# Kernel optimization log

Hardware: AMD Instinct MI355X
Metric: run time of the kernel (lower is better)

Reference implementation:

```python
import jax, jax.numpy as jnp
import numpy as np

DEPTH = 6; HEADS = 6; DIM = 384; HD = DIM // HEADS
WS = 14; WINDOW_BLOCKS = (0, 1, 3, 4)
IMG = 512; PATCH = 16; GRID = IMG // PATCH        # 32x32 token grid
PRE_GRID = 14                                      # 224 // 16 pretrain grid
SCALE = HD ** -0.5


def layer_norm(x, w, b, eps=1e-5):
    u = x.mean(-1, keepdims=True)
    s = ((x - u) ** 2).mean(-1, keepdims=True)
    return (x - u) / jnp.sqrt(s + eps) * w + b


def get_rel_pos(size, rel_pos):
    # q_size == k_size here; relative coords in [0, 2*size-2]
    coords = jnp.arange(size)[:, None] - jnp.arange(size)[None, :] + (size - 1)
    return rel_pos[coords]  # (size, size, HD)


def attention(x, qkv_w, qkv_b, proj_w, proj_b, rel_h, rel_w):
    B, H, W, C = x.shape
    N = H * W
    qkv = (x.reshape(B, N, C) @ qkv_w.T + qkv_b).reshape(B, N, 3, HEADS, HD)
    qkv = jnp.moveaxis(qkv, 2, 0).transpose(0, 1, 3, 2, 4)  # (3,B,h,N,d)
    q, k, v = qkv[0], qkv[1], qkv[2]
    attn = jnp.einsum('bhqd,bhkd->bhqk', q * SCALE, k)
    # decomposed relative position bias (ViTDet add_decomposed_rel_pos)
    Rh = get_rel_pos(H, rel_h)  # (H,H,d)
    Rw = get_rel_pos(W, rel_w)  # (W,W,d)
    rq = q.reshape(B, HEADS, H, W, HD)
    bias_h = jnp.einsum('bnhwc,hkc->bnhwk', rq, Rh)  # (B,h,H,W,H)
    bias_w = jnp.einsum('bnhwc,wkc->bnhwk', rq, Rw)  # (B,h,H,W,W)
    attn = (attn.reshape(B, HEADS, H, W, H, W)
            + bias_h[..., :, None] + bias_w[..., None, :]).reshape(B, HEADS, N, N)
    attn = jax.nn.softmax(attn, axis=-1)
    out = jnp.einsum('bhqk,bhkd->bhqd', attn, v)
    out = out.transpose(0, 2, 1, 3).reshape(B, H, W, C)
    return out @ proj_w.T + proj_b


def window_partition(x, ws):
    B, H, W, C = x.shape
    pad_h = (ws - H % ws) % ws
    pad_w = (ws - W % ws) % ws
    x = jnp.pad(x, ((0, 0), (0, pad_h), (0, pad_w), (0, 0)))
    Hp, Wp = H + pad_h, W + pad_w
    x = x.reshape(B, Hp // ws, ws, Wp // ws, ws, C)
    x = x.transpose(0, 1, 3, 2, 4, 5).reshape(-1, ws, ws, C)
    return x, Hp, Wp


def window_unpartition(win, ws, Hp, Wp, H, W):
    B = win.shape[0] // ((Hp // ws) * (Wp // ws))
    x = win.reshape(B, Hp // ws, Wp // ws, ws, ws, -1)
    x = x.transpose(0, 1, 3, 2, 4, 5).reshape(B, Hp, Wp, -1)
    return x[:, :H, :W]


def block(x, p, windowed):
    shortcut = x
    x = layer_norm(x, p['n1w'], p['n1b'])
    if windowed:
        H, W = x.shape[1], x.shape[2]
        x, Hp, Wp = window_partition(x, WS)
    x = attention(x, p['qw'], p['qb'], p['pw'], p['pb'], p['rh'], p['rw'])
    if windowed:
        x = window_unpartition(x, WS, Hp, Wp, H, W)
    x = shortcut + x
    h = layer_norm(x, p['n2w'], p['n2b'])
    h = jax.nn.gelu(h @ p['f1w'].T + p['f1b'], approximate=False)
    return x + h @ p['f2w'].T + p['f2b']


def vit_forward(x, patch_w, patch_b, pos_embed, norm1_w, norm1_b, qkv_w, qkv_b,
                proj_w, proj_b, norm2_w, norm2_b, fc1_w, fc1_b, fc2_w, fc2_b,
                rel_pos_h, rel_pos_w):
    y = jax.lax.conv_general_dilated(
        x, patch_w, (PATCH, PATCH), 'VALID',
        dimension_numbers=('NCHW', 'OIHW', 'NCHW'))
    y = y.transpose(0, 2, 3, 1) + patch_b  # (B, GRID, GRID, DIM)
    # abs pos embed: bicubic resize from pretrain 14x14 grid to 32x32
    pos = pos_embed.reshape(1, PRE_GRID, PRE_GRID, DIM)
    pos = jax.image.resize(pos, (1, GRID, GRID, DIM), 'bicubic')
    y = y + pos
    for i in range(DEPTH):
        windowed = i in WINDOW_BLOCKS
        L = 2 * WS - 1 if windowed else 2 * GRID - 1
        p = dict(n1w=norm1_w[i], n1b=norm1_b[i], qw=qkv_w[i], qb=qkv_b[i],
                 pw=proj_w[i], pb=proj_b[i], rh=rel_pos_h[i, :L], rw=rel_pos_w[i, :L],
                 n2w=norm2_w[i], n2b=norm2_b[i], f1w=fc1_w[i], f1b=fc1_b[i],
                 f2w=fc2_w[i], f2b=fc2_b[i])
        y = block(y, p, windowed)
    return y.transpose(0, 3, 1, 2)  # (B, DIM, GRID, GRID) 'last_feat'


def setup_inputs() -> dict:
    key = jax.random.key(0)
    ks = jax.random.split(key, 10)
    B = 4
    std = 0.02
    f32 = jnp.float32
    return {
        'x': jax.random.normal(ks[0], (B, 3, IMG, IMG), f32),
        'patch_w': jax.random.normal(ks[1], (DIM, 3, PATCH, PATCH), f32) * 0.05,
        'patch_b': jnp.zeros((DIM,), f32),
        'pos_embed': jax.random.normal(ks[2], (1, PRE_GRID * PRE_GRID, DIM), f32) * std,
        'norm1_w': jnp.ones((DEPTH, DIM), f32),
        'norm1_b': jnp.zeros((DEPTH, DIM), f32),
        'qkv_w': jax.random.normal(ks[3], (DEPTH, 3 * DIM, DIM), f32) * std,
        'qkv_b': jnp.zeros((DEPTH, 3 * DIM), f32),
        'proj_w': jax.random.normal(ks[4], (DEPTH, DIM, DIM), f32) * std,
        'proj_b': jnp.zeros((DEPTH, DIM), f32),
        'norm2_w': jnp.ones((DEPTH, DIM), f32),
        'norm2_b': jnp.zeros((DEPTH, DIM), f32),
        'fc1_w': jax.random.normal(ks[5], (DEPTH, 4 * DIM, DIM), f32) * std,
        'fc1_b': jnp.zeros((DEPTH, 4 * DIM), f32),
        'fc2_w': jax.random.normal(ks[6], (DEPTH, DIM, 4 * DIM), f32) * std,
        'fc2_b': jnp.zeros((DEPTH, DIM), f32),
        'rel_pos_h': jax.random.normal(ks[7], (DEPTH, 2 * GRID - 1, HD), f32) * std,
        'rel_pos_w': jax.random.normal(ks[8], (DEPTH, 2 * GRID - 1, HD), f32) * std,
    }


def reference(x, patch_w, patch_b, pos_embed, norm1_w, norm1_b, qkv_w, qkv_b,
              proj_w, proj_b, norm2_w, norm2_b, fc1_w, fc1_b, fc2_w, fc2_b,
              rel_pos_h, rel_pos_w):
    return vit_forward(x, patch_w, patch_b, pos_embed, norm1_w, norm1_b, qkv_w, qkv_b,
                       proj_w, proj_b, norm2_w, norm2_b, fc1_w, fc1_b, fc2_w, fc2_b,
                       rel_pos_h, rel_pos_w)
```

## Files before the change

kernel.cpp:

```cpp
#include <hip/hip_runtime.h>
#include <math.h>

#define B_SZ 4
#define DIM 384
#define HEADS 6
#define HD 64
#define NTOK 4096
#define WS 14
#define NWIN 36
#define WTOK 196

typedef unsigned short u16;
typedef __bf16 bf16_t;
typedef bf16_t bf16x8 __attribute__((ext_vector_type(8)));
typedef float f32x4 __attribute__((ext_vector_type(4)));

__device__ __forceinline__ float bf2f(unsigned u) { return __uint_as_float(u << 16); }
__device__ __forceinline__ u16 f2bf(float f) {
    unsigned u = __float_as_uint(f);
    unsigned r = (u + 0x7fffu + ((u >> 16) & 1u)) >> 16;
    return (u16)r;
}

__device__ __forceinline__ void ldsload16(const u16* g, u16* l) {
    __builtin_amdgcn_global_load_lds(
        (const __attribute__((address_space(1))) unsigned int*)g,
        (__attribute__((address_space(3))) unsigned int*)l, 16, 0, 0);
}

__device__ __forceinline__ int swz(int r) { return (r ^ (r >> 2)) & 3; }

__device__ inline float cubic_keys(float x) {
    x = fabsf(x);
    if (x <= 1.f) return ((1.5f * x - 2.5f) * x) * x + 1.f;
    if (x < 2.f)  return ((-0.5f * x + 2.5f) * x - 4.f) * x + 2.f;
    return 0.f;
}

__global__ __launch_bounds__(256) void setup_kernel(
        const float* __restrict__ p0, const float* __restrict__ p1,
        const float* __restrict__ p2, const float* __restrict__ p3,
        const float* __restrict__ p4, const float* __restrict__ p5,
        u16* __restrict__ wb, const float* __restrict__ pe,
        float* __restrict__ posr, const float* __restrict__ x,
        u16* __restrict__ col) {
    int i = blockIdx.x * 256 + threadIdx.x;
    if (i < 10918656) {
        const float* s; int off;
        if      (i <   294912) { s = p0; off = 0; }
        else if (i <  2949120) { s = p1; off = 294912; }
        else if (i <  3833856) { s = p2; off = 2949120; }
        else if (i <  7372800) { s = p3; off = 3833856; }
        else if (i < 10911744) { s = p4; off = 7372800; }
        else                   { s = p5; off = 10911744; }
        wb[i] = f2bf(s[i - off]);
        return;
    }
    i -= 10918656;
    if (i < 393216) {
        int c = i % 384;
        int g = i / 384;
        int gy = g / 32, gx = g % 32;
        float wy[14], wx[14];
        float sy = (gy + 0.5f) * (14.f / 32.f) - 0.5f;
        float sx = (gx + 0.5f) * (14.f / 32.f) - 0.5f;
        float toty = 0.f, totx = 0.f;
        #pragma unroll
        for (int k = 0; k < 14; ++k) {
            wy[k] = cubic_keys(sy - (float)k); toty += wy[k];
            wx[k] = cubic_keys(sx - (float)k); totx += wx[k];
        }
        float val = 0.f;
        #pragma unroll 1
        for (int iy = 0; iy < 14; ++iy) {
            if (wy[iy] == 0.f) continue;
            float row = 0.f;
            for (int ix = 0; ix < 14; ++ix) {
                if (wx[ix] == 0.f) continue;
                row += wx[ix] * pe[(iy * 14 + ix) * 384 + c];
            }
            val += wy[iy] * row;
        }
        posr[i] = val / (toty * totx);
        return;
    }
    i -= 393216;
    {
        int kk = i % 768;
        int p  = i / 768;
        int b  = p / 1024;
        int ph = (p % 1024) / 32;
        int pw = p % 32;
        int c = kk / 256;
        int r = kk % 256;
        int ii = r / 16, j = r % 16;
        col[i] = f2bf(x[(size_t)b * 3 * 512 * 512 + (size_t)c * 512 * 512 +
                        (size_t)(ph * 16 + ii) * 512 + (pw * 16 + j)]);
    }
}

__global__ __launch_bounds__(64) void epi_ln_kernel(const float* __restrict__ P,
        const float* __restrict__ bias, const float* __restrict__ posr,
        float* __restrict__ y, int addy, int nsk,
        const float* __restrict__ lw, const float* __restrict__ lb,
        u16* __restrict__ lnout, float* __restrict__ outT)
{
    int tok = blockIdx.x, t = threadIdx.x;
    size_t base = (size_t)tok * 384;
    float v[6];
    float s = 0.f;
    #pragma unroll
    for (int i = 0; i < 6; ++i) {
        int c = t + 64 * i;
        float val = bias[c];
        #pragma unroll 1
        for (int sk = 0; sk < nsk; ++sk)
            val += P[(size_t)sk * 1572864 + base + c];
        if (posr) val += posr[(size_t)(tok & 1023) * 384 + c];
        if (addy) val += y[base + c];
        v[i] = val; s += val;
    }
    if (outT) {
        int b = tok >> 10, g = tok & 1023;
        #pragma unroll
        for (int i = 0; i < 6; ++i) {
            int c = t + 64 * i;
            outT[((size_t)(b * 384 + c)) * 1024 + g] = v[i];
        }
        return;
    }
    #pragma unroll
    for (int i = 0; i < 6; ++i) y[base + t + 64 * i] = v[i];
    if (!lnout) return;
    #pragma unroll
    for (int off = 32; off > 0; off >>= 1) s += __shfl_xor(s, off);
    float mean = s * (1.f / 384.f);
    float vs = 0.f;
    #pragma unroll
    for (int i = 0; i < 6; ++i) { float d = v[i] - mean; vs += d * d; }
    #pragma unroll
    for (int off = 32; off > 0; off >>= 1) vs += __shfl_xor(vs, off);
    float inv = rsqrtf(vs * (1.f / 384.f) + 1e-5f);
    u16* orow = lnout + base;
    #pragma unroll
    for (int i = 0; i < 6; ++i) {
        int c = t + 64 * i;
        orow[c] = f2bf((v[i] - mean) * inv * lw[c] + lb[c]);
    }
}

__global__ __launch_bounds__(256) void mfma_gemm3(
        const u16* __restrict__ A, const u16* __restrict__ Wt,
        const float* __restrict__ bias,
        float* __restrict__ outf, u16* __restrict__ outb,
        float* __restrict__ outp,
        int M, int N, int K, int act, int ksplit)
{
    __shared__ u16 As[8192];
    __shared__ u16 Bs[4096];
    int t = threadIdx.x;
    int lane = t & 63, wave = t >> 6;
    int wm = (wave >> 1) * 64, wn = (wave & 1) * 32;
    int m0 = blockIdx.y * 128, n0 = blockIdx.x * 64;
    int ks = blockIdx.z * ksplit, ke = ks + ksplit;

    int r0 = t >> 2,        c0 = ((t & 3) ^ swz(t >> 2)) * 8;
    int r1 = 64 + (t >> 2), c1 = ((t & 3) ^ swz(64 + (t >> 2))) * 8;
    const u16* a0 = A + (size_t)(m0 + r0) * K + c0;
    const u16* a1 = A + (size_t)(m0 + r1) * K + c1;
    const u16* b0 = Wt + (size_t)(n0 + r0) * K + c0;
    u16* asd0 = &As[wave * 512];
    u16* asd1 = &As[2048 + wave * 512];
    u16* bsd0 = &Bs[wave * 512];

    f32x4 acc[4][2] = {};
    int row_a = wm + (lane & 15);
    int row_b = wn + (lane & 15);
    int lq = lane >> 4;

    for (int k0 = ks; k0 < ke; k0 += 64) {
        ldsload16(a0 + k0, asd0);
        ldsload16(a1 + k0, asd1);
        ldsload16(b0 + k0, bsd0);
        ldsload16(a0 + k0 + 32, asd0 + 4096);
        ldsload16(a1 + k0 + 32, asd1 + 4096);
        ldsload16(b0 + k0 + 32, bsd0 + 2048);
        __syncthreads();
        #pragma unroll
        for (int hf = 0; hf < 2; ++hf) {
            bf16x8 af[4], bfr[2];
            #pragma unroll
            for (int i = 0; i < 4; ++i) {
                int r = row_a + i * 16;
                af[i] = *(const bf16x8*)&As[hf * 4096 + r * 32 + ((lq ^ swz(r)) * 8)];
            }
            #pragma unroll
            for (int j = 0; j < 2; ++j) {
                int r = row_b + j * 16;
                bfr[j] = *(const bf16x8*)&Bs[hf * 2048 + r * 32 + ((lq ^ swz(r)) * 8)];
            }
            #pragma unroll
            for (int i = 0; i < 4; ++i)
                #pragma unroll
                for (int j = 0; j < 2; ++j)
                    acc[i][j] = __builtin_amdgcn_mfma_f32_16x16x32_bf16(
                        af[i], bfr[j], acc[i][j], 0, 0, 0);
        }
        __syncthreads();
    }

    int colq = lane & 15, rowq = (lane >> 4) * 4;
    if (outp) {
        float* pp = outp + (size_t)blockIdx.z * M * N;
        #pragma unroll
        for (int i = 0; i < 4; ++i) {
            #pragma unroll
            for (int rr = 0; rr < 4; ++rr) {
                int m = m0 + wm + i * 16 + rowq + rr;
                size_t mo = (size_t)m * N;
                #pragma unroll
                for (int j = 0; j < 2; ++j) {
                    int n = n0 + wn + j * 16 + colq;
                    pp[mo + n] = acc[i][j][rr];
                }
            }
        }
        return;
    }
    #pragma unroll
    for (int i = 0; i < 4; ++i) {
        #pragma unroll
        for (int rr = 0; rr < 4; ++rr) {
            int m = m0 + wm + i * 16 + rowq + rr;
            size_t mo = (size_t)m * N;
            #pragma unroll
            for (int j = 0; j < 2; ++j) {
                int n = n0 + wn + j * 16 + colq;
                float v = acc[i][j][rr] + bias[n];
                if (act)  v = 0.5f * v * (1.f + erff(v * 0.70710678118654752f));
                if (outf) outf[mo + n] = v;
                if (outb) outb[mo + n] = f2bf(v);
            }
        }
    }
}

template<int N, int W>
__global__ __launch_bounds__(256) void attn_mfma(const u16* __restrict__ qkv,
        const u16* __restrict__ qkb, const float* __restrict__ rh,
        const float* __restrict__ rw, u16* __restrict__ outb)
{
    constexpr int JS = (W == 32) ? 64 : 32;
    constexpr int L  = (W == 32) ? 63 : 27;
    constexpr int CTR = W - 1;
    __shared__ u16 KV[11776];
    __shared__ u16 bhl[64 * 66];
    __shared__ u16 bwl[64 * 66];
    __shared__ u16 Qt[64 * 66];

    u16* Pb = KV + 9216;
    u16* Rt = KV;

    int t = threadIdx.x, lane = t & 63, wave = t >> 6;
    int quad = lane >> 4, l15 = lane & 15;
    int uh = blockIdx.x, qb0 = blockIdx.y * 64;
    int h = uh % HEADS, u = uh / HEADS;
    size_t tbase = (size_t)u * 1024;
    int wb_ = u / 9, wr = u - wb_ * 9;
    int wy = wr / 3, wx = wr - wy * 3;

    auto rowptr = [&](int lq2) -> const u16* {
        if constexpr (W == 32) {
            return qkv + (tbase + lq2) * 1152;
        } else {
            int iy = lq2 / WS, ix = lq2 - iy * WS;
            int gy = wy * WS + iy, gx = wx * WS + ix;
            if (gy < 32 && gx < 32)
                return qkv + (size_t)(wb_ * 1024 + gy * 32 + gx) * 1152;
            return qkb;
        }
    };

    {
        int q = t & 63, ch0 = (t >> 6) * 16;
        int qc = qb0 + q; if (qc >= N) qc = N - 1;
        const u16* qp = rowptr(qc) + h * 64 + ch0;
        uint4 a = *(const uint4*)qp;
        uint4 b = *(const uint4*)(qp + 8);
        u16 vals[16];
        *(uint4*)vals = a; *(uint4*)(vals + 8) = b;
        #pragma unroll
        for (int c = 0; c < 16; ++c)
            Qt[(ch0 + c) * 66 + q] = ((qb0 + q) < N) ? vals[c] : (u16)0;
    }

    #pragma unroll
    for (int table = 0; table < 2; ++table) {
        __syncthreads();
        const float* tab = table ? rw : rh;
        for (int idx = t; idx < JS * 8; idx += 256) {
            int j = idx >> 3, cc0 = (idx & 7) * 8;
            u16 tmp[8];
            if (j < L) {
                const float* src = tab + (size_t)j * 64 + cc0;
                #pragma unroll
                for (int c = 0; c < 8; ++c) tmp[c] = f2bf(src[c]);
            } else {
                #pragma unroll
                for (int c = 0; c < 8; ++c) tmp[c] = 0;
            }
            *(uint4*)&Rt[j * 72 + cc0] = *(uint4*)tmp;
        }
        __syncthreads();
        if (wave < JS / 16) {
            int jt = wave;
            bf16x8 af0 = *(const bf16x8*)&Rt[(jt * 16 + l15) * 72 + quad * 8];
            bf16x8 af1 = *(const bf16x8*)&Rt[(jt * 16 + l15) * 72 + 32 + quad * 8];
            u16* dst = table ? bwl : bhl;
            #pragma unroll
            for (int qt = 0; qt < 4; ++qt) {
                bf16x8 qf0, qf1;
                u16* p0 = (u16*)&qf0; u16* p1 = (u16*)&qf1;
                #pragma unroll
                for (int z = 0; z < 8; ++z) {
                    p0[z] = Qt[(quad * 8 + z) * 66 + qt * 16 + l15];
                    p1[z] = Qt[(32 + quad * 8 + z) * 66 + qt * 16 + l15];
                }
                f32x4 acc = {};
                acc = __builtin_amdgcn_mfma_f32_16x16x32_bf16(af0, qf0, acc, 0, 0, 0);
                acc = __builtin_amdgcn_mfma_f32_16x16x32_bf16(af1, qf1, acc, 0, 0, 0);
                #pragma unroll
                for (int r = 0; r < 4; ++r)
                    dst[(qt * 16 + l15) * 66 + jt * 16 + quad * 4 + r] = f2bf(acc[r]);
            }
        }
    }
    __syncthreads();

    constexpr int NKT = (N + 31) / 32;
    {
        int pch = wave * 64 + lane;
        int key = pch >> 3;
        int c8 = (pch & 7) ^ (key & 7);
        int kc = key; if (kc >= N) kc = N - 1;
        ldsload16(rowptr(kc) + 384 + h * 64 + c8 * 8, KV + wave * 512);
        int k = t & 31, ch0v = (t >> 5) * 8;
        uint4 vv = *(const uint4*)(rowptr(k) + 768 + h * 64 + ch0v);
        u16 tmp[8]; *(uint4*)tmp = vv;
        u16* vdst = KV + 4096;
        #pragma unroll
        for (int c = 0; c < 8; ++c) vdst[(ch0v + c) * 40 + k] = tmp[c];
    }

    bf16x8 qf[2];
    #pragma unroll
    for (int hc = 0; hc < 2; ++hc) {
        u16* qv = (u16*)&qf[hc];
        #pragma unroll
        for (int j = 0; j < 8; ++j)
            qv[j] = Qt[(hc * 32 + quad * 8 + j) * 66 + wave * 16 + l15];
    }
    int qme = wave * 16 + l15;
    int qq = qb0 + qme; if (qq >= N) qq = N - 1;
    int qh = qq / W, qw = qq - qh * W;
    float bwreg[2][4];
    if constexpr (W == 32) {
        #pragma unroll
        for (int kc2 = 0; kc2 < 2; ++kc2)
            #pragma unroll
            for (int r = 0; r < 4; ++r) {
                int keyl = kc2 * 16 + quad * 4 + r;
                bwreg[kc2][r] = bf2f(bwl[qme * 66 + (qw - keyl + CTR)]);
            }
    }

    f32x4 of[4] = {};
    float lsum = 0.f;
    __syncthreads();

    for (int kt = 0; kt < NKT; ++kt) {
        int kb = kt * 32;
        int p = kt & 1;
        const u16* ksp = KV + p * 2048;
        const u16* vtp = KV + 4096 + p * 2560;
        bool pref = (kt + 1 < NKT);
        uint4 vpref;
        int kpf = t & 31, ch0v = (t >> 5) * 8;
        if (pref) {
            int kb2 = kb + 32;
            int pch = wave * 64 + lane;
            int key = pch >> 3;
            int c8 = (pch & 7) ^ (key & 7);
            int kc = kb2 + key; if (kc >= N) kc = N - 1;
            ldsload16(rowptr(kc) + 384 + h * 64 + c8 * 8,
                      KV + (1 - p) * 2048 + wave * 512);
            int kcv = kb2 + kpf; if (kcv >= N) kcv = N - 1;
            vpref = *(const uint4*)(rowptr(kcv) + 768 + h * 64 + ch0v);
        }

        f32x4 st[2] = {};
        #pragma unroll
        for (int hc = 0; hc < 2; ++hc) {
            #pragma unroll
            for (int kc2 = 0; kc2 < 2; ++kc2) {
                int key = kc2 * 16 + l15;
                int c8 = hc * 4 + quad;
                int pp = key * 8 + (c8 ^ (key & 7));
                bf16x8 kf = *(const bf16x8*)&ksp[pp * 8];
                st[kc2] = __builtin_amdgcn_mfma_f32_16x16x32_bf16(
                    kf, qf[hc], st[kc2], 0, 0, 0);
            }
        }
        float bh_t = 0.f;
        if constexpr (W == 32) bh_t = bf2f(bhl[qme * 66 + (qh - (kb >> 5) + CTR)]);
        #pragma unroll
        for (int kc2 = 0; kc2 < 2; ++kc2) {
            #pragma unroll
            for (int r = 0; r < 4; ++r) {
                int keyl = kc2 * 16 + quad * 4 + r;
                int key = kb + keyl;
                float b;
                if constexpr (W == 32) {
                    b = bh_t + bwreg[kc2][r];
                } else {
                    int kk2 = (key < N) ? key : (N - 1);
                    int kh = kk2 / W, kw = kk2 - kh * W;
                    b = bf2f(bhl[qme * 66 + (qh - kh + CTR)]) +
                        bf2f(bwl[qme * 66 + (qw - kw + CTR)]);
                }
                float pv = __expf(fmaf(st[kc2][r], 0.125f, b));
                if (key >= N) pv = 0.f;
                lsum += pv;
                Pb[wave * 640 + l15 * 40 + keyl] = f2bf(pv);
            }
        }
        bf16x8 pf = *(const bf16x8*)&Pb[wave * 640 + l15 * 40 + quad * 8];
        #pragma unroll
        for (int ca = 0; ca < 4; ++ca) {
            bf16x8 vf = *(const bf16x8*)&vtp[(ca * 16 + l15) * 40 + quad * 8];
            of[ca] = __builtin_amdgcn_mfma_f32_16x16x32_bf16(
                vf, pf, of[ca], 0, 0, 0);
        }

        if (pref) {
            u16 tmp[8]; *(uint4*)tmp = vpref;
            u16* vdst = KV + 4096 + (1 - p) * 2560;
            #pragma unroll
            for (int c = 0; c < 8; ++c) vdst[(ch0v + c) * 40 + kpf] = tmp[c];
            __syncthreads();
        }
    }

    lsum += __shfl_xor(lsum, 16);
    lsum += __shfl_xor(lsum, 32);
    float inv = 1.f / lsum;
    int q = qb0 + qme;
    if (q < N) {
        u16* op;
        if constexpr (W == 32) {
            op = outb + (tbase + q) * 384 + h * 64;
        } else {
            int iy = q / WS, ix = q - iy * WS;
            int gy = wy * WS + iy, gx = wx * WS + ix;
            if (gy >= 32 || gx >= 32) return;
            op = outb + (size_t)(wb_ * 1024 + gy * 32 + gx) * 384 + h * 64;
        }
        #pragma unroll
        for (int ca = 0; ca < 4; ++ca)
            #pragma unroll
            for (int r = 0; r < 4; ++r)
                op[ca * 16 + quad * 4 + r] = f2bf(of[ca][r] * inv);
    }
}

static inline void launch_gemm(const u16* A, const u16* W, const float* bias,
                               float* outf, u16* outb,
                               int M, int N, int K, int act, hipStream_t s) {
    dim3 g(N / 64, M / 128, 1);
    mfma_gemm3<<<g, 256, 0, s>>>(A, W, bias, outf, outb, nullptr, M, N, K, act, K);
}

static inline void launch_gemm_sk(const u16* A, const u16* W, float* P,
                                  int M, int N, int K, int SK, hipStream_t s) {
    dim3 g(N / 64, M / 128, SK);
    mfma_gemm3<<<g, 256, 0, s>>>(A, W, nullptr, nullptr, nullptr, P,
                                 M, N, K, 0, K / SK);
}

extern "C" void kernel_launch(void* const* d_in, const int* in_sizes, int n_in,
                              void* d_out, int out_size, void* d_ws, size_t ws_size,
                              hipStream_t stream) {
    const float* x      = (const float*)d_in[0];
    const float* patchw = (const float*)d_in[1];
    const float* patchb = (const float*)d_in[2];
    const float* pos    = (const float*)d_in[3];
    const float* n1w    = (const float*)d_in[4];
    const float* n1b    = (const float*)d_in[5];
    const float* qkvw   = (const float*)d_in[6];
    const float* qkvb   = (const float*)d_in[7];
    const float* pw     = (const float*)d_in[8];
    const float* pb     = (const float*)d_in[9];
    const float* n2w    = (const float*)d_in[10];
    const float* n2b    = (const float*)d_in[11];
    const float* f1w    = (const float*)d_in[12];
    const float* f1b    = (const float*)d_in[13];
    const float* f2w    = (const float*)d_in[14];
    const float* f2b    = (const float*)d_in[15];
    const float* rph    = (const float*)d_in[16];
    const float* rpw    = (const float*)d_in[17];
    float* out = (float*)d_out;

    float* y   = (float*)d_ws;
    u16* attb  = (u16*)(y + 1572864);
    u16* mlpb  = attb + 1572864;
    u16* lnb   = mlpb + 6291456;
    u16* qkvx  = lnb + 1572864;
    u16* rsrv  = qkvx + 4718592;
    u16* wb    = rsrv + 7864320;
    float* posr = (float*)(wb + 10918656);

    u16* colb  = rsrv;
    float* P_patch = (float*)attb;
    float* P_pf    = (float*)qkvx;

    u16* wb_patch = wb;
    u16* wb_qkv   = wb + 294912;
    u16* wb_pw    = wb + 2949120;
    u16* wb_f1    = wb + 3833856;
    u16* wb_f2    = wb + 7372800;
    u16* wqb      = wb + 10911744;

    setup_kernel<<<(14457600 + 255) / 256, 256, 0, stream>>>(
        patchw, qkvw, pw, f1w, f2w, qkvb, wb, pos, posr, x, colb);

    launch_gemm_sk(colb, wb_patch, P_patch, NTOK, 384, 768, 2, stream);
    epi_ln_kernel<<<NTOK, 64, 0, stream>>>(P_patch, patchb, posr, y, 0, 2,
                                           n1w, n1b, lnb, nullptr);

    for (int i = 0; i < 6; ++i) {
        bool windowed = (i == 0 || i == 1 || i == 3 || i == 4);
        const float* rh = rph + (size_t)i * 63 * 64;
        const float* rw = rpw + (size_t)i * 63 * 64;
        launch_gemm(lnb, wb_qkv + (size_t)i * 442368, qkvb + i * 1152,
                    nullptr, qkvx, NTOK, 1152, 384, 0, stream);
        if (windowed) {
            attn_mfma<WTOK, WS><<<dim3(NWIN * HEADS, 4), 256, 0, stream>>>(
                qkvx, wqb + i * 1152, rh, rw, attb);
        } else {
            attn_mfma<1024, 32><<<dim3(B_SZ * HEADS, 16), 256, 0, stream>>>(
                qkvx, wqb + i * 1152, rh, rw, attb);
        }
        launch_gemm_sk(attb, wb_pw + (size_t)i * 147456, P_pf,
                       NTOK, 384, 384, 2, stream);
        epi_ln_kernel<<<NTOK, 64, 0, stream>>>(P_pf, pb + i * 384, nullptr, y, 1, 2,
                                               n2w + i * 384, n2b + i * 384, lnb,
                                               nullptr);
        launch_gemm(lnb, wb_f1 + (size_t)i * 589824, f1b + i * 1536,
                    nullptr, mlpb, NTOK, 1536, 384, 1, stream);
        launch_gemm_sk(mlpb, wb_f2 + (size_t)i * 589824, P_pf,
                       NTOK, 384, 1536, 2, stream);
        if (i < 5)
            epi_ln_kernel<<<NTOK, 64, 0, stream>>>(P_pf, f2b + i * 384, nullptr, y,
                                                   1, 2, n1w + (i + 1) * 384,
                                                   n1b + (i + 1) * 384, lnb, nullptr);
        else
            epi_ln_kernel<<<NTOK, 64, 0, stream>>>(P_pf, f2b + i * 384, nullptr, y,
                                                   1, 2, nullptr, nullptr, nullptr,
                                                   out);
    }
}
```

Before: 775.6 us.

## Double-buffer GEMM LDS tiles and vectorize setup conversions by four

The GEMM now uses two LDS buffers, so the next K-chunk is loaded while MFMAs run on the current one, and one barrier per iteration is removed. The setup kernel handles four elements per thread with float4 loads and packed bf16 stores for weight conversion, pos-embed resize and im2col. The aim is to hide global-load latency in every GEMM and to cut memory instructions in setup. Doubling LDS per block may lower occupancy.

```diff
diff --git a/kernel.cpp b/kernel.cpp
--- a/kernel.cpp
+++ b/kernel.cpp
@@ -44,7 +44,7 @@
         u16* __restrict__ wb, const float* __restrict__ pe,
         float* __restrict__ posr, const float* __restrict__ x,
         u16* __restrict__ col) {
-    int i = blockIdx.x * 256 + threadIdx.x;
+    int i = (blockIdx.x * 256 + threadIdx.x) * 4;
     if (i < 10918656) {
         const float* s; int off;
         if      (i <   294912) { s = p0; off = 0; }
@@ -53,7 +53,9 @@
         else if (i <  7372800) { s = p3; off = 3833856; }
         else if (i < 10911744) { s = p4; off = 7372800; }
         else                   { s = p5; off = 10911744; }
-        wb[i] = f2bf(s[i - off]);
+        float4 v = *(const float4*)(s + (i - off));
+        u16 o[4] = { f2bf(v.x), f2bf(v.y), f2bf(v.z), f2bf(v.w) };
+        *(uint2*)(wb + i) = *(const uint2*)o;
         return;
     }
     i -= 10918656;
@@ -70,22 +72,27 @@
             wy[k] = cubic_keys(sy - (float)k); toty += wy[k];
             wx[k] = cubic_keys(sx - (float)k); totx += wx[k];
         }
-        float val = 0.f;
+        float4 acc = {0.f, 0.f, 0.f, 0.f};
         #pragma unroll 1
         for (int iy = 0; iy < 14; ++iy) {
             if (wy[iy] == 0.f) continue;
-            float row = 0.f;
+            float4 row = {0.f, 0.f, 0.f, 0.f};
             for (int ix = 0; ix < 14; ++ix) {
                 if (wx[ix] == 0.f) continue;
-                row += wx[ix] * pe[(iy * 14 + ix) * 384 + c];
-            }
-            val += wy[iy] * row;
-        }
-        posr[i] = val / (toty * totx);
+                float4 pv = *(const float4*)(pe + (iy * 14 + ix) * 384 + c);
+                row.x += wx[ix] * pv.x; row.y += wx[ix] * pv.y;
+                row.z += wx[ix] * pv.z; row.w += wx[ix] * pv.w;
+            }
+            acc.x += wy[iy] * row.x; acc.y += wy[iy] * row.y;
+            acc.z += wy[iy] * row.z; acc.w += wy[iy] * row.w;
+        }
+        float inv = 1.f / (toty * totx);
+        acc.x *= inv; acc.y *= inv; acc.z *= inv; acc.w *= inv;
+        *(float4*)(posr + i) = acc;
         return;
     }
     i -= 393216;
-    {
+    if (i < 3145728) {
         int kk = i % 768;
         int p  = i / 768;
         int b  = p / 1024;
@@ -94,8 +101,11 @@
         int c = kk / 256;
         int r = kk % 256;
         int ii = r / 16, j = r % 16;
-        col[i] = f2bf(x[(size_t)b * 3 * 512 * 512 + (size_t)c * 512 * 512 +
-                        (size_t)(ph * 16 + ii) * 512 + (pw * 16 + j)]);
+        float4 v = *(const float4*)(x + (size_t)b * 3 * 512 * 512 +
+                                    (size_t)c * 512 * 512 +
+                                    (size_t)(ph * 16 + ii) * 512 + (pw * 16 + j));
+        u16 o[4] = { f2bf(v.x), f2bf(v.y), f2bf(v.z), f2bf(v.w) };
+        *(uint2*)(col + i) = *(const uint2*)o;
     }
 }
 
@@ -149,55 +159,61 @@
     }
 }
 
-__global__ __launch_bounds__(256) void mfma_gemm3(
+__global__ __launch_bounds__(256) void mfma_gemm4(
         const u16* __restrict__ A, const u16* __restrict__ Wt,
         const float* __restrict__ bias,
         float* __restrict__ outf, u16* __restrict__ outb,
         float* __restrict__ outp,
         int M, int N, int K, int act, int ksplit)
 {
-    __shared__ u16 As[8192];
-    __shared__ u16 Bs[4096];
+    __shared__ u16 As[2][8192];
+    __shared__ u16 Bs[2][4096];
     int t = threadIdx.x;
     int lane = t & 63, wave = t >> 6;
     int wm = (wave >> 1) * 64, wn = (wave & 1) * 32;
     int m0 = blockIdx.y * 128, n0 = blockIdx.x * 64;
-    int ks = blockIdx.z * ksplit, ke = ks + ksplit;
+    int ks = blockIdx.z * ksplit;
 
     int r0 = t >> 2,        c0 = ((t & 3) ^ swz(t >> 2)) * 8;
     int r1 = 64 + (t >> 2), c1 = ((t & 3) ^ swz(64 + (t >> 2))) * 8;
     const u16* a0 = A + (size_t)(m0 + r0) * K + c0;
     const u16* a1 = A + (size_t)(m0 + r1) * K + c1;
     const u16* b0 = Wt + (size_t)(n0 + r0) * K + c0;
-    u16* asd0 = &As[wave * 512];
-    u16* asd1 = &As[2048 + wave * 512];
-    u16* bsd0 = &Bs[wave * 512];
+
+    auto stage = [&](int k0, int buf) {
+        ldsload16(a0 + k0,      &As[buf][wave * 512]);
+        ldsload16(a1 + k0,      &As[buf][2048 + wave * 512]);
+        ldsload16(b0 + k0,      &Bs[buf][wave * 512]);
+        ldsload16(a0 + k0 + 32, &As[buf][4096 + wave * 512]);
+        ldsload16(a1 + k0 + 32, &As[buf][6144 + wave * 512]);
+        ldsload16(b0 + k0 + 32, &Bs[buf][2048 + wave * 512]);
+    };
 
     f32x4 acc[4][2] = {};
     int row_a = wm + (lane & 15);
     int row_b = wn + (lane & 15);
     int lq = lane >> 4;
-
-    for (int k0 = ks; k0 < ke; k0 += 64) {
-        ldsload16(a0 + k0, asd0);
-        ldsload16(a1 + k0, asd1);
-        ldsload16(b0 + k0, bsd0);
-        ldsload16(a0 + k0 + 32, asd0 + 4096);
-        ldsload16(a1 + k0 + 32, asd1 + 4096);
-        ldsload16(b0 + k0 + 32, bsd0 + 2048);
-        __syncthreads();
+    int nchunks = ksplit / 64;
+
+    stage(ks, 0);
+    __syncthreads();
+
+    for (int ci = 0; ci < nchunks; ++ci) {
+        int p = ci & 1;
+        bool pref = (ci + 1 < nchunks);
+        if (pref) stage(ks + (ci + 1) * 64, 1 - p);
         #pragma unroll
         for (int hf = 0; hf < 2; ++hf) {
             bf16x8 af[4], bfr[2];
             #pragma unroll
             for (int i = 0; i < 4; ++i) {
                 int r = row_a + i * 16;
-                af[i] = *(const bf16x8*)&As[hf * 4096 + r * 32 + ((lq ^ swz(r)) * 8)];
+                af[i] = *(const bf16x8*)&As[p][hf * 4096 + r * 32 + ((lq ^ swz(r)) * 8)];
             }
             #pragma unroll
             for (int j = 0; j < 2; ++j) {
                 int r = row_b + j * 16;
-                bfr[j] = *(const bf16x8*)&Bs[hf * 2048 + r * 32 + ((lq ^ swz(r)) * 8)];
+                bfr[j] = *(const bf16x8*)&Bs[p][hf * 2048 + r * 32 + ((lq ^ swz(r)) * 8)];
             }
             #pragma unroll
             for (int i = 0; i < 4; ++i)
@@ -206,7 +222,7 @@
                     acc[i][j] = __builtin_amdgcn_mfma_f32_16x16x32_bf16(
                         af[i], bfr[j], acc[i][j], 0, 0, 0);
         }
-        __syncthreads();
+        if (pref) __syncthreads();
     }
 
     int colq = lane & 15, rowq = (lane >> 4) * 4;
@@ -477,13 +493,13 @@
                                float* outf, u16* outb,
                                int M, int N, int K, int act, hipStream_t s) {
     dim3 g(N / 64, M / 128, 1);
-    mfma_gemm3<<<g, 256, 0, s>>>(A, W, bias, outf, outb, nullptr, M, N, K, act, K);
+    mfma_gemm4<<<g, 256, 0, s>>>(A, W, bias, outf, outb, nullptr, M, N, K, act, K);
 }
 
 static inline void launch_gemm_sk(const u16* A, const u16* W, float* P,
                                   int M, int N, int K, int SK, hipStream_t s) {
     dim3 g(N / 64, M / 128, SK);
-    mfma_gemm3<<<g, 256, 0, s>>>(A, W, nullptr, nullptr, nullptr, P,
+    mfma_gemm4<<<g, 256, 0, s>>>(A, W, nullptr, nullptr, nullptr, P,
                                  M, N, K, 0, K / SK);
 }
 
@@ -530,7 +546,7 @@
     u16* wb_f2    = wb + 7372800;
     u16* wqb      = wb + 10911744;
 
-    setup_kernel<<<(14457600 + 255) / 256, 256, 0, stream>>>(
+    setup_kernel<<<(14457600 / 4 + 255) / 256, 256, 0, stream>>>(
         patchw, qkvw, pw, f1w, f2w, qkvb, wb, pos, posr, x, colb);
 
     launch_gemm_sk(colb, wb_patch, P_patch, NTOK, 384, 768, 2, stream);
```

After: 762.6 us. No clear change (-1.7%).
